# Performance work log

Measured on AMD Instinct MI355X. Metric: run time of the kernel, lower is better.

## Reference

```python
import jax, jax.numpy as jnp
import numpy as np

N_EMBD = 1024
N_HEAD = 16
HEAD_SIZE = N_EMBD // N_HEAD


def setup_inputs() -> dict:
    key = jax.random.key(0)
    k1, k2, k3, k4 = jax.random.split(key, 4)
    x = jax.random.normal(k1, (2, 2048, N_EMBD), dtype=jnp.float32)
    # nn.Linear weights: stored as [out, in]; apply as x @ W.T
    scale = 1.0 / np.sqrt(N_EMBD)
    W_kqv = jax.random.uniform(k2, (3 * N_EMBD, N_EMBD), jnp.float32, -scale, scale)
    W_proj = jax.random.uniform(k3, (N_EMBD, N_EMBD), jnp.float32, -scale, scale)
    b_proj = jax.random.uniform(k4, (N_EMBD,), jnp.float32, -scale, scale)
    return {"x": x, "W_kqv": W_kqv, "W_proj": W_proj, "b_proj": b_proj}


def reference(x, W_kqv, W_proj, b_proj):
    B, T, C = x.shape
    H, D = N_HEAD, HEAD_SIZE
    kqv = x @ W_kqv.T  # [B, T, 3C]
    # source splits as k, q, v (k first)
    k, q, v = jnp.split(kqv, 3, axis=-1)
    k = k.reshape(B, T, H, D).transpose(0, 2, 1, 3)  # [B,H,T,D]
    q = q.reshape(B, T, H, D).transpose(0, 2, 1, 3)
    v = v.reshape(B, T, H, D).transpose(0, 2, 1, 3)
    wei = jnp.einsum('bhqd,bhkd->bhqk', q, k) * (D ** -0.5)  # [B,H,T,T]
    causal = jnp.tril(jnp.ones((T, T), dtype=bool))
    wei = jnp.where(causal[None, None], wei, -jnp.inf)
    wei = jax.nn.softmax(wei, axis=-1)
    out = jnp.einsum('bhqk,bhkd->bhqd', wei, v)  # [B,H,T,D]
    out = out.transpose(0, 2, 1, 3).reshape(B, T, C)
    return out @ W_proj.T + b_proj
```

## Files before the change

### kernel.cpp

```cpp
#include <hip/hip_runtime.h>
#include <cstdint>


typedef __bf16 bf16x8 __attribute__((ext_vector_type(8)));
typedef unsigned short u16x8 __attribute__((ext_vector_type(8)));
typedef float f32x4 __attribute__((ext_vector_type(4)));

__device__ __forceinline__ float bf2f(unsigned short u) {
    return __uint_as_float(((unsigned int)u) << 16);
}
__device__ __forceinline__ unsigned short f2bf(float f) {
    unsigned int u = __float_as_uint(f);
    u += 0x7fffu + ((u >> 16) & 1u);
    return (unsigned short)(u >> 16);
}
__device__ __forceinline__ void stC(float* p, float v) { *p = v; }
__device__ __forceinline__ void stC(unsigned short* p, float v) { *p = f2bf(v); }

__device__ __forceinline__ void gl2lds16(const unsigned short* g, unsigned short* l) {
    __builtin_amdgcn_global_load_lds(
        (__attribute__((address_space(1))) void*)g,
        (__attribute__((address_space(3))) void*)l, 16, 0, 0);
}

__device__ __forceinline__ unsigned short* swz(unsigned short* base, int row, int col) {
    const int off = ((row << 7) + (col << 1)) ^ ((row & 7) << 4);
    return (unsigned short*)((char*)base + off);
}
__device__ __forceinline__ const unsigned short* swz(const unsigned short* base, int row, int col) {
    const int off = ((row << 7) + (col << 1)) ^ ((row & 7) << 4);
    return (const unsigned short*)((const char*)base + off);
}

__device__ __forceinline__ void cvt8(const float* __restrict__ s, unsigned short* __restrict__ d) {
    const f32x4 a = *(const f32x4*)s;
    const f32x4 b = *(const f32x4*)(s + 4);
    u16x8 o;
    o[0] = f2bf(a[0]); o[1] = f2bf(a[1]); o[2] = f2bf(a[2]); o[3] = f2bf(a[3]);
    o[4] = f2bf(b[0]); o[5] = f2bf(b[1]); o[6] = f2bf(b[2]); o[7] = f2bf(b[3]);
    *(u16x8*)d = o;
}
__global__ __launch_bounds__(256) void cvt_bf16_3(
    const float* __restrict__ s0, unsigned short* __restrict__ d0, int n0,
    const float* __restrict__ s1, unsigned short* __restrict__ d1, int n1,
    const float* __restrict__ s2, unsigned short* __restrict__ d2, int n2)
{
    const int t = blockIdx.x * 256 + threadIdx.x;
    const int S = gridDim.x * 256;
    for (int i = t; i < n0 / 8; i += S) cvt8(s0 + (size_t)i * 8, d0 + (size_t)i * 8);
    for (int i = t; i < n1 / 8; i += S) cvt8(s1 + (size_t)i * 8, d1 + (size_t)i * 8);
    for (int i = t; i < n2 / 8; i += S) cvt8(s2 + (size_t)i * 8, d2 + (size_t)i * 8);
}

__global__ __launch_bounds__(256, 3) void gemm_qkv(
    const unsigned short* __restrict__ A, const unsigned short* __restrict__ B,
    unsigned short* __restrict__ C, int M, int N, int K)
{
    __shared__ __align__(16) unsigned short As[128 * 64];
    __shared__ __align__(16) unsigned short Bs[128 * 64];

    const int tid = threadIdx.x;
    const int bn = blockIdx.x, bm = blockIdx.y;
    const int w = tid >> 6, lane = tid & 63;
    const int quad = lane >> 4, l16 = lane & 15;
    const int wm = (w >> 1) * 64, wn = (w & 1) * 64;

    f32x4 acc[4][4] = {};

    const int srow = (lane >> 3);
    const int scol = ((lane & 7) ^ srow) * 8;
    const unsigned short* Ag = &A[(size_t)(bm * 128 + w * 32 + srow) * K + scol];
    const unsigned short* Bg = &B[(size_t)(bn * 128 + w * 32 + srow) * K + scol];
    unsigned short* AsW = &As[(w * 32) * 64];
    unsigned short* BsW = &Bs[(w * 32) * 64];

    for (int k0 = 0; k0 < K; k0 += 64) {
#pragma unroll
        for (int i = 0; i < 4; i++) {
            gl2lds16(Ag + (size_t)(i * 8) * K + k0, AsW + i * 8 * 64);
            gl2lds16(Bg + (size_t)(i * 8) * K + k0, BsW + i * 8 * 64);
        }
        __syncthreads();

#pragma unroll
        for (int ks = 0; ks < 2; ks++) {
            bf16x8 af[4], bfr[4];
#pragma unroll
            for (int t = 0; t < 4; t++) {
                af[t]  = *(const bf16x8*)swz(As, wm + t * 16 + l16, ks * 32 + quad * 8);
                bfr[t] = *(const bf16x8*)swz(Bs, wn + t * 16 + l16, ks * 32 + quad * 8);
            }
#pragma unroll
            for (int mt = 0; mt < 4; mt++)
#pragma unroll
                for (int nt = 0; nt < 4; nt++)
                    acc[mt][nt] = __builtin_amdgcn_mfma_f32_16x16x32_bf16(
                        af[mt], bfr[nt], acc[mt][nt], 0, 0, 0);
        }
        __syncthreads();
    }

#pragma unroll
    for (int mt = 0; mt < 4; mt++) {
        const int row = bm * 128 + wm + mt * 16 + quad * 4;
#pragma unroll
        for (int nt = 0; nt < 4; nt++) {
            const int col = bn * 128 + wn + nt * 16 + l16;
#pragma unroll
            for (int r = 0; r < 4; r++)
                stC(&C[(size_t)(row + r) * N + col], acc[mt][nt][r]);
        }
    }
}

__global__ __launch_bounds__(256) void gemm_proj(
    const unsigned short* __restrict__ A, const unsigned short* __restrict__ B,
    const float* __restrict__ bias, float* __restrict__ C, int M, int N, int K)
{
    __shared__ __align__(16) unsigned short As[64 * 32];
    __shared__ __align__(16) unsigned short Bs[128 * 32];

    const int tid = threadIdx.x;
    const int bn = blockIdx.x, bm = blockIdx.y;
    const int w = tid >> 6, lane = tid & 63;
    const int quad = lane >> 4, l16 = lane & 15;
    const int wm = (w >> 1) * 32, wn = (w & 1) * 64;

    f32x4 acc[2][4] = {};

    const int srow = w * 16 + (lane >> 2);
    const int scol = (lane & 3) * 8;
    const unsigned short* Ag = &A[(size_t)(bm * 64 + srow) * K + scol];
    const unsigned short* Bg = &B[(size_t)(bn * 128 + srow) * K + scol];
    unsigned short* AsW = &As[(w * 16) * 32];
    unsigned short* BsW = &Bs[(w * 16) * 32];

    for (int k0 = 0; k0 < K; k0 += 32) {
        gl2lds16(Ag + k0, AsW);
        gl2lds16(Bg + k0, BsW);
        gl2lds16(Bg + (size_t)64 * K + k0, BsW + 64 * 32);
        __syncthreads();

        bf16x8 af[2], bfr[4];
#pragma unroll
        for (int t = 0; t < 2; t++)
            af[t]  = *(const bf16x8*)&As[(wm + t * 16 + l16) * 32 + quad * 8];
#pragma unroll
        for (int t = 0; t < 4; t++)
            bfr[t] = *(const bf16x8*)&Bs[(wn + t * 16 + l16) * 32 + quad * 8];
#pragma unroll
        for (int mt = 0; mt < 2; mt++)
#pragma unroll
            for (int nt = 0; nt < 4; nt++)
                acc[mt][nt] = __builtin_amdgcn_mfma_f32_16x16x32_bf16(
                    af[mt], bfr[nt], acc[mt][nt], 0, 0, 0);
        __syncthreads();
    }

#pragma unroll
    for (int mt = 0; mt < 2; mt++) {
        const int row = bm * 64 + wm + mt * 16 + quad * 4;
#pragma unroll
        for (int nt = 0; nt < 4; nt++) {
            const int col = bn * 128 + wn + nt * 16 + l16;
            const float bv = bias[col];
#pragma unroll
            for (int r = 0; r < 4; r++)
                C[(size_t)(row + r) * N + col] = acc[mt][nt][r] + bv;
        }
    }
}

__global__ __launch_bounds__(256) void attn_fused(
    const unsigned short* __restrict__ kqv,
    unsigned short* __restrict__ out)
{
    __shared__ __align__(16) unsigned short Qs[64 * 64];
    __shared__ __align__(16) unsigned short Ks[2][64 * 64];
    __shared__ __align__(16) unsigned short Vts[2][64 * 64];
    __shared__ __align__(16) unsigned short Ps[64 * 64];

    const int bh = blockIdx.x;
    const int qt = 31 - (int)blockIdx.y;
    const int b = bh >> 4, h = bh & 15;
    const int tid = threadIdx.x;
    const int w = tid >> 6;
    const int lane = tid & 63;
    const int quad = lane >> 4, l16 = lane & 15;
    const int rowBase = b * 2048;
    const int kOff = h * 64, qOff = 1024 + h * 64, vOff = 2048 + h * 64;
    const float SEXP = 0.125f * 1.4426950408889634f;
    const float MASKV = -1.0e30f;

#pragma unroll
    for (int i = 0; i < 2; i++) {
        const int v = tid + i * 256;
        const int row = v >> 3, c8 = (v & 7) * 8;
        *(u16x8*)swz(Qs, row, c8) =
            *(const u16x8*)&kqv[(size_t)(rowBase + qt * 64 + row) * 3072 + qOff + c8];
    }

    f32x4 o[4] = {};
    float l_i[4] = {0.f, 0.f, 0.f, 0.f};

    u16x8 kr[2], vr[2];
#pragma unroll
    for (int i = 0; i < 2; i++) {
        const int v = tid + i * 256;
        kr[i] = *(const u16x8*)&kqv[(size_t)(rowBase + (v >> 3)) * 3072 + kOff + (v & 7) * 8];
        vr[i] = *(const u16x8*)&kqv[(size_t)(rowBase + lane) * 3072 + vOff + (i * 4 + w) * 8];
    }

    for (int j = 0; j <= qt; j++) {
        const int cur = j & 1;
#pragma unroll
        for (int i = 0; i < 2; i++) {
            const int v = tid + i * 256;
            *(u16x8*)swz(Ks[cur], v >> 3, (v & 7) * 8) = kr[i];
            const int d8 = i * 4 + w;
#pragma unroll
            for (int u = 0; u < 8; u++)
                *swz(Vts[cur], d8 * 8 + u, lane) = vr[i][u];
        }
        __syncthreads();

        if (j < qt) {
#pragma unroll
            for (int i = 0; i < 2; i++) {
                const int v = tid + i * 256;
                kr[i] = *(const u16x8*)&kqv[(size_t)(rowBase + (j + 1) * 64 + (v >> 3)) * 3072 + kOff + (v & 7) * 8];
                vr[i] = *(const u16x8*)&kqv[(size_t)(rowBase + (j + 1) * 64 + lane) * 3072 + vOff + (i * 4 + w) * 8];
            }
        }

        f32x4 s[4] = {};
#pragma unroll
        for (int ks = 0; ks < 2; ks++) {
            const bf16x8 aq = *(const bf16x8*)swz(Qs, w * 16 + l16, ks * 32 + quad * 8);
#pragma unroll
            for (int nt = 0; nt < 4; nt++) {
                const bf16x8 bk = *(const bf16x8*)swz(Ks[cur], nt * 16 + l16, ks * 32 + quad * 8);
                s[nt] = __builtin_amdgcn_mfma_f32_16x16x32_bf16(aq, bk, s[nt], 0, 0, 0);
            }
        }

        if (j == qt) {
            const int rowl = w * 16 + quad * 4;
#pragma unroll
            for (int nt = 0; nt < 4; nt++) {
                const int coll = nt * 16 + l16;
#pragma unroll
                for (int r = 0; r < 4; r++)
                    if (coll > rowl + r) s[nt][r] = MASKV;
            }
        }

#pragma unroll
        for (int nt = 0; nt < 4; nt++) {
#pragma unroll
            for (int r = 0; r < 4; r++) {
                const float p = exp2f(s[nt][r] * SEXP);
                l_i[r] += p;
                *swz(Ps, w * 16 + quad * 4 + r, nt * 16 + l16) = f2bf(p);
            }
        }

#pragma unroll
        for (int ks = 0; ks < 2; ks++) {
            const bf16x8 ap = *(const bf16x8*)swz(Ps, w * 16 + l16, ks * 32 + quad * 8);
#pragma unroll
            for (int nt = 0; nt < 4; nt++) {
                const bf16x8 bv = *(const bf16x8*)swz(Vts[cur], nt * 16 + l16, ks * 32 + quad * 8);
                o[nt] = __builtin_amdgcn_mfma_f32_16x16x32_bf16(ap, bv, o[nt], 0, 0, 0);
            }
        }
    }

    float linv[4];
#pragma unroll
    for (int r = 0; r < 4; r++) {
        float t = l_i[r];
        t += __shfl_xor(t, 1);
        t += __shfl_xor(t, 2);
        t += __shfl_xor(t, 4);
        t += __shfl_xor(t, 8);
        linv[r] = 1.0f / t;
    }

#pragma unroll
    for (int nt = 0; nt < 4; nt++) {
        const int col = h * 64 + nt * 16 + l16;
#pragma unroll
        for (int r = 0; r < 4; r++)
            out[(size_t)(rowBase + qt * 64 + w * 16 + quad * 4 + r) * 1024 + col] =
                f2bf(o[nt][r] * linv[r]);
    }
}

extern "C" void kernel_launch(void* const* d_in, const int* in_sizes, int n_in,
                              void* d_out, int out_size, void* d_ws, size_t ws_size,
                              hipStream_t stream) {
    const float* x     = (const float*)d_in[0];
    const float* Wkqv  = (const float*)d_in[1];
    const float* Wproj = (const float*)d_in[2];
    const float* bproj = (const float*)d_in[3];
    float* out = (float*)d_out;

    unsigned short* kqv    = (unsigned short*)d_ws;
    unsigned short* attn   = kqv    + (size_t)4096 * 3072;
    unsigned short* xb     = attn   + (size_t)4096 * 1024;
    unsigned short* wkqvb  = xb     + (size_t)4096 * 1024;
    unsigned short* wprojb = wkqvb  + (size_t)3072 * 1024;

    cvt_bf16_3<<<dim3(512), dim3(256), 0, stream>>>(
        x, xb, 4096 * 1024, Wkqv, wkqvb, 3072 * 1024, Wproj, wprojb, 1024 * 1024);

    gemm_qkv<<<dim3(24, 32), dim3(256), 0, stream>>>(
        xb, wkqvb, kqv, 4096, 3072, 1024);

    attn_fused<<<dim3(32, 32), dim3(256), 0, stream>>>(kqv, attn);

    gemm_proj<<<dim3(8, 64), dim3(256), 0, stream>>>(
        attn, wprojb, bproj, out, 4096, 1024, 1024);
}
```

Before: 182.8 us.

## Rewrite QKV GEMM with 256x256 tiles, 8 waves, double-buffered LDS pipeline

The QKV projection GEMM moves from 128x128 tiles with 4 waves and a single LDS buffer to 256x256 tiles with 8 waves and double-buffered LDS. Global-to-LDS loads for the next K-tile are interleaved across four sub-phases, each fenced by explicit barriers, waitcnts and sched_barriers, so that loads overlap MFMA work. The aim is to cut per-tile synchronisation stalls and raise data reuse per block. In exchange the grid shrinks to 192 blocks, which may underfill the GPU's 256 CUs, and register pressure rises with 32 accumulators per thread. A __syncthreads is also added in the attention kernel between writing P to LDS and reading it back, which looks like a race fix.

```diff
diff --git a/kernel.cpp b/kernel.cpp
--- a/kernel.cpp
+++ b/kernel.cpp
@@ -52,63 +52,132 @@
     for (int i = t; i < n2 / 8; i += S) cvt8(s2 + (size_t)i * 8, d2 + (size_t)i * 8);
 }
 
-__global__ __launch_bounds__(256, 3) void gemm_qkv(
+template <int P>
+__device__ __forceinline__ void mfmaq(f32x4 (&acc)[8][4],
+                                      const bf16x8 (&af)[2][2],
+                                      const bf16x8 (&bfr)[4][2]) {
+#pragma unroll
+    for (int m2 = 0; m2 < 2; m2++)
+#pragma unroll
+        for (int nt = 0; nt < 4; nt++)
+#pragma unroll
+            for (int ks = 0; ks < 2; ks++)
+                acc[2 * P + m2][nt] = __builtin_amdgcn_mfma_f32_16x16x32_bf16(
+                    af[m2][ks], bfr[nt][ks], acc[2 * P + m2][nt], 0, 0, 0);
+}
+
+__global__ __launch_bounds__(512) void gemm_qkv(
     const unsigned short* __restrict__ A, const unsigned short* __restrict__ B,
     unsigned short* __restrict__ C, int M, int N, int K)
 {
-    __shared__ __align__(16) unsigned short As[128 * 64];
-    __shared__ __align__(16) unsigned short Bs[128 * 64];
+    __shared__ __align__(16) unsigned short As[2][256 * 64];
+    __shared__ __align__(16) unsigned short Bs[2][256 * 64];
 
     const int tid = threadIdx.x;
     const int bn = blockIdx.x, bm = blockIdx.y;
     const int w = tid >> 6, lane = tid & 63;
     const int quad = lane >> 4, l16 = lane & 15;
-    const int wm = (w >> 1) * 64, wn = (w & 1) * 64;
-
-    f32x4 acc[4][4] = {};
-
-    const int srow = (lane >> 3);
-    const int scol = ((lane & 7) ^ srow) * 8;
-    const unsigned short* Ag = &A[(size_t)(bm * 128 + w * 32 + srow) * K + scol];
-    const unsigned short* Bg = &B[(size_t)(bn * 128 + w * 32 + srow) * K + scol];
-    unsigned short* AsW = &As[(w * 32) * 64];
-    unsigned short* BsW = &Bs[(w * 32) * 64];
-
-    for (int k0 = 0; k0 < K; k0 += 64) {
-#pragma unroll
-        for (int i = 0; i < 4; i++) {
-            gl2lds16(Ag + (size_t)(i * 8) * K + k0, AsW + i * 8 * 64);
-            gl2lds16(Bg + (size_t)(i * 8) * K + k0, BsW + i * 8 * 64);
-        }
-        __syncthreads();
-
-#pragma unroll
-        for (int ks = 0; ks < 2; ks++) {
-            bf16x8 af[4], bfr[4];
-#pragma unroll
-            for (int t = 0; t < 4; t++) {
-                af[t]  = *(const bf16x8*)swz(As, wm + t * 16 + l16, ks * 32 + quad * 8);
-                bfr[t] = *(const bf16x8*)swz(Bs, wn + t * 16 + l16, ks * 32 + quad * 8);
-            }
-#pragma unroll
-            for (int mt = 0; mt < 4; mt++)
-#pragma unroll
-                for (int nt = 0; nt < 4; nt++)
-                    acc[mt][nt] = __builtin_amdgcn_mfma_f32_16x16x32_bf16(
-                        af[mt], bfr[nt], acc[mt][nt], 0, 0, 0);
-        }
-        __syncthreads();
-    }
-
-#pragma unroll
-    for (int mt = 0; mt < 4; mt++) {
-        const int row = bm * 128 + wm + mt * 16 + quad * 4;
+    const int wm = (w >> 2) * 128, wn = (w & 3) * 64;
+    const int NT = K >> 6;
+
+    f32x4 acc[8][4] = {};
+
+    const int srow8 = lane >> 3;
+    const int scol = ((lane & 7) ^ srow8) * 8;
+    const unsigned short* Ab = A + (size_t)bm * 256 * K;
+    const unsigned short* Bb = B + (size_t)bn * 256 * K;
+
+    auto stage = [&](const unsigned short* __restrict__ G, unsigned short* lds,
+                     int tT, int hh) {
+#pragma unroll
+        for (int i = 0; i < 2; i++) {
+            const int r = hh * 128 + w * 16 + i * 8;
+            gl2lds16(G + (size_t)(r + srow8) * K + tT * 64 + scol, lds + r * 64);
+        }
+    };
+    auto ldA = [&](bf16x8 (&af)[2][2], const unsigned short* AsB, int p) {
+#pragma unroll
+        for (int m2 = 0; m2 < 2; m2++)
+#pragma unroll
+            for (int ks = 0; ks < 2; ks++)
+                af[m2][ks] = *(const bf16x8*)swz(AsB, wm + p * 32 + m2 * 16 + l16,
+                                                 ks * 32 + quad * 8);
+    };
+    auto ldB = [&](bf16x8 (&bf_)[4][2], const unsigned short* BsB) {
+#pragma unroll
+        for (int nt = 0; nt < 4; nt++)
+#pragma unroll
+            for (int ks = 0; ks < 2; ks++)
+                bf_[nt][ks] = *(const bf16x8*)swz(BsB, wn + nt * 16 + l16,
+                                                  ks * 32 + quad * 8);
+    };
+
+    stage(Bb, Bs[0], 0, 0); stage(Bb, Bs[0], 0, 1);
+    stage(Ab, As[0], 0, 0); stage(Ab, As[0], 0, 1);
+    stage(Bb, Bs[1], 1, 0); stage(Bb, Bs[1], 1, 1);
+    asm volatile("s_waitcnt vmcnt(4)" ::: "memory");
+    __builtin_amdgcn_s_barrier();
+
+    for (int t = 0; t < NT; t++) {
+        const unsigned short* AsB = As[t & 1];
+        const unsigned short* BsB = Bs[t & 1];
+        unsigned short* AsN = As[(t + 1) & 1];
+        unsigned short* BsN = Bs[t & 1];
+        bf16x8 bfr[4][2];
+        {
+            bf16x8 af[2][2];
+            ldA(af, AsB, 0);
+            ldB(bfr, BsB);
+            if (t + 1 < NT) stage(Ab, AsN, t + 1, 0);
+            __builtin_amdgcn_s_barrier();
+            asm volatile("s_waitcnt lgkmcnt(0)" ::: "memory");
+            __builtin_amdgcn_sched_barrier(0);
+            mfmaq<0>(acc, af, bfr);
+            __builtin_amdgcn_s_barrier();
+        }
+        {
+            bf16x8 af[2][2];
+            ldA(af, AsB, 1);
+            if (t + 1 < NT) stage(Ab, AsN, t + 1, 1);
+            if (t + 2 < NT) stage(Bb, BsN, t + 2, 0);
+            __builtin_amdgcn_s_barrier();
+            asm volatile("s_waitcnt lgkmcnt(0)" ::: "memory");
+            __builtin_amdgcn_sched_barrier(0);
+            mfmaq<1>(acc, af, bfr);
+            __builtin_amdgcn_s_barrier();
+        }
+        {
+            bf16x8 af[2][2];
+            ldA(af, AsB, 2);
+            if (t + 2 < NT) stage(Bb, BsN, t + 2, 1);
+            __builtin_amdgcn_s_barrier();
+            asm volatile("s_waitcnt lgkmcnt(0)" ::: "memory");
+            __builtin_amdgcn_sched_barrier(0);
+            mfmaq<2>(acc, af, bfr);
+            __builtin_amdgcn_s_barrier();
+        }
+        {
+            bf16x8 af[2][2];
+            ldA(af, AsB, 3);
+            if (t < NT - 2)       asm volatile("s_waitcnt vmcnt(4)" ::: "memory");
+            else if (t == NT - 2) asm volatile("s_waitcnt vmcnt(0)" ::: "memory");
+            __builtin_amdgcn_s_barrier();
+            asm volatile("s_waitcnt lgkmcnt(0)" ::: "memory");
+            __builtin_amdgcn_sched_barrier(0);
+            mfmaq<3>(acc, af, bfr);
+            __builtin_amdgcn_s_barrier();
+        }
+    }
+
+#pragma unroll
+    for (int mf = 0; mf < 8; mf++) {
+        const int row = bm * 256 + wm + mf * 16 + quad * 4;
 #pragma unroll
         for (int nt = 0; nt < 4; nt++) {
-            const int col = bn * 128 + wn + nt * 16 + l16;
+            const int col = bn * 256 + wn + nt * 16 + l16;
 #pragma unroll
             for (int r = 0; r < 4; r++)
-                stC(&C[(size_t)(row + r) * N + col], acc[mt][nt][r]);
+                C[(size_t)(row + r) * N + col] = f2bf(acc[mf][nt][r]);
         }
     }
 }
@@ -264,6 +333,7 @@
                 *swz(Ps, w * 16 + quad * 4 + r, nt * 16 + l16) = f2bf(p);
             }
         }
+        __syncthreads();
 
 #pragma unroll
         for (int ks = 0; ks < 2; ks++) {
@@ -315,7 +385,7 @@
     cvt_bf16_3<<<dim3(512), dim3(256), 0, stream>>>(
         x, xb, 4096 * 1024, Wkqv, wkqvb, 3072 * 1024, Wproj, wprojb, 1024 * 1024);
 
-    gemm_qkv<<<dim3(24, 32), dim3(256), 0, stream>>>(
+    gemm_qkv<<<dim3(12, 16), dim3(512), 0, stream>>>(
         xb, wkqvb, kqv, 4096, 3072, 1024);
 
     attn_fused<<<dim3(32, 32), dim3(256), 0, stream>>>(kqv, attn);
```

Result: no change. 182.9 us (+0.1%).
